# Performance work log

Measured on AMD Instinct MI355X. Metric: run time of the kernel, lower is better.

## Reference

```python
import jax, jax.numpy as jnp
import numpy as np
import math

B, T, F, H = 8, 1024, 512, 8
DK = F // H

def setup_inputs() -> dict:
    key = jax.random.key(0)
    ks = jax.random.split(key, 14)
    s = 0.02
    return {
        "query": jax.random.normal(ks[0], (B, T, F), jnp.float32),
        "key_in": jax.random.normal(ks[1], (B, T, F), jnp.float32),
        "value": jax.random.normal(ks[2], (B, T, F), jnp.float32),
        "pos_emb": jax.random.normal(ks[3], (1, 2 * T - 1, F), jnp.float32),
        "mask": jnp.ones((B, 1, T), jnp.int32),
        "Wq": jax.random.normal(ks[4], (F, F), jnp.float32) * s,
        "bq": jnp.zeros((F,), jnp.float32),
        "Wk": jax.random.normal(ks[5], (F, F), jnp.float32) * s,
        "bk": jnp.zeros((F,), jnp.float32),
        "Wv": jax.random.normal(ks[6], (F, F), jnp.float32) * s,
        "bv": jnp.zeros((F,), jnp.float32),
        "Wo": jax.random.normal(ks[7], (F, F), jnp.float32) * s,
        "bo": jnp.zeros((F,), jnp.float32),
        "Wp": jax.random.normal(ks[8], (F, F), jnp.float32) * s,
        "pos_bias_u": jax.random.normal(ks[9], (H, DK), jnp.float32) * s,
        "pos_bias_v": jax.random.normal(ks[10], (H, DK), jnp.float32) * s,
    }

def _rel_shift(x):
    # x: [B,H,T1, 2*T1-1] -> Transformer-XL pad/reshape trick -> [B,H,T1,T1]
    b, h, t1, n = x.shape
    zero_pad = jnp.zeros((b, h, t1, 1), x.dtype)
    x_padded = jnp.concatenate([zero_pad, x], axis=-1)  # [B,H,T1,n+1]
    x_padded = x_padded.reshape(b, h, n + 1, t1)
    x = x_padded[:, :, 1:].reshape(b, h, t1, n)
    return x[..., : n // 2 + 1]

def reference(query, key_in, value, pos_emb, mask,
              Wq, bq, Wk, bk, Wv, bv, Wo, bo, Wp, pos_bias_u, pos_bias_v):
    b, t1, f = query.shape
    # qkv projections -> [B,T,H,DK]
    q = (query @ Wq.T + bq).reshape(b, t1, H, DK)
    k = (key_in @ Wk.T + bk).reshape(b, -1, H, DK)
    v = (value @ Wv.T + bv).reshape(b, -1, H, DK)
    # positional projection (batch 1) -> [P,H,DK]
    p = (pos_emb @ Wp.T).reshape(pos_emb.shape[1], H, DK)
    q_u = q + pos_bias_u  # broadcast [H,DK]
    q_v = q + pos_bias_v
    matrix_ac = jnp.einsum("bthd,bshd->bhts", q_u, k)
    matrix_bd = jnp.einsum("bthd,phd->bhtp", q_v, p)
    matrix_bd = _rel_shift(matrix_bd)
    scores = (matrix_ac + matrix_bd) / math.sqrt(DK)  # [B,H,T,T]
    neg = jnp.finfo(scores.dtype).min
    m = (mask[:, None, :, :] == 0)  # [B,1,1,T] or [B,1,T,T]
    scores = jnp.where(m, neg, scores)
    attn = jax.nn.softmax(scores, axis=-1)
    attn = jnp.where(m, 0.0, attn)
    x = jnp.einsum("bhts,bshd->bthd", attn, v).reshape(b, t1, H * DK)
    return x @ Wo.T + bo
```

## Files before the change

### kernel.cpp

```cpp
#include <hip/hip_runtime.h>
#include <math.h>

#define T_SEQ 1024
#define FEAT  512
#define NH    8
#define DKH   64

typedef __attribute__((ext_vector_type(8))) short          bf16x8;
typedef _Float16 f16;
typedef __attribute__((ext_vector_type(8))) _Float16       f16x8;
typedef __attribute__((ext_vector_type(4))) float          f32x4;
typedef __attribute__((ext_vector_type(8))) unsigned short u16x8;
typedef __attribute__((ext_vector_type(4))) unsigned short u16x4;

__device__ __forceinline__ float bf2f(unsigned short u) {
    union { unsigned int i; float f; } x; x.i = ((unsigned int)u) << 16; return x.f;
}
__device__ __forceinline__ unsigned short f2bf(float f) {
    union { float f; unsigned int i; } x; x.f = f;
    unsigned int r = x.i + 0x7FFFu + ((x.i >> 16) & 1u);
    return (unsigned short)(r >> 16);
}
__device__ __forceinline__ unsigned short f2h_bits(float f) {
    const f16 h = (f16)f;
    union { f16 h; unsigned short u; } x; x.h = h; return x.u;
}

typedef const __attribute__((address_space(1))) unsigned int* gas_ptr;
typedef __attribute__((address_space(3))) unsigned int*       las_ptr;
__device__ __forceinline__ void glds16(const unsigned short* g, unsigned short* l) {
    __builtin_amdgcn_global_load_lds((gas_ptr)(const void*)g, (las_ptr)(void*)l, 16, 0, 0);
}

struct SplitPack {
    const float*    src[9];
    unsigned short* hi[9];
    unsigned short* lo[9];
    int             n4[9];
};

__global__ __launch_bounds__(256)
void split_f32(SplitPack pk) {
    const int ten = blockIdx.y;
    const int n4  = pk.n4[ten];
    const float4* s = (const float4*)pk.src[ten];
    u16x4* dh = (u16x4*)pk.hi[ten];
    u16x4* dl = (u16x4*)pk.lo[ten];
    for (int i = blockIdx.x * blockDim.x + threadIdx.x; i < n4;
         i += gridDim.x * blockDim.x) {
        const float4 v = s[i];
        float a[4] = {v.x, v.y, v.z, v.w};
        u16x4 h, l;
#pragma unroll
        for (int j = 0; j < 4; ++j) {
            h[j] = f2bf(a[j]);
            l[j] = f2bf(a[j] - bf2f(h[j]));
        }
        dh[i] = h; dl[i] = l;
    }
}

#define GBUF 12288

template<int OUTMODE>
__global__ __launch_bounds__(256)
void gemm_ps(const unsigned short* __restrict__ Agh,
             const unsigned short* __restrict__ Agl,
             const unsigned short* __restrict__ Wh,
             const unsigned short* __restrict__ Wl,
             const float* __restrict__ bias,
             void* __restrict__ Cout, int M, int N, int K)
{
    __shared__ unsigned short lds[2 * GBUF];

    const int tid  = threadIdx.x;
    const int w    = tid >> 6, lane = tid & 63, g = lane >> 4, c = lane & 15;
    const int m0   = blockIdx.x * 128, n0 = blockIdx.y * 64;
    const int wr   = (w >> 1) * 64, wc = (w & 1) * 32;

    f32x4 acc[4][2];
#pragma unroll
    for (int m = 0; m < 4; ++m)
#pragma unroll
        for (int n = 0; n < 2; ++n)
#pragma unroll
            for (int r = 0; r < 4; ++r) acc[m][n][r] = 0.f;

    auto STAGE = [&](unsigned short* base, int kc) {
        const int k0 = kc * 32;
#pragma unroll
        for (int q = 0; q < 2; ++q) {
            const int chunk = q * 256 + w * 64 + lane;
            const int row = chunk >> 2, p = chunk & 3;
            const int gra = m0 + row;
            const int gr  = (gra < M) ? gra : (M - 1);
            const size_t go = (size_t)gr * K + k0 + p * 8;
            glds16(Agh + go, base + chunk * 8);
            glds16(Agl + go, base + 4096 + chunk * 8);
        }
        {
            const int chunk = w * 64 + lane;
            const int row = chunk >> 2, p = chunk & 3;
            const size_t go = (size_t)(n0 + row) * K + k0 + p * 8;
            glds16(Wh + go, base + 8192 + chunk * 8);
            glds16(Wl + go, base + 10240 + chunk * 8);
        }
    };

    STAGE(lds, 0);
    __syncthreads();

    const int nk = K / 32;
    int cur = 0;
    for (int kc = 0; kc < nk; ++kc) {
        if (kc + 1 < nk) STAGE(lds + (cur ^ 1) * GBUF, kc + 1);

        const unsigned short* Bs = lds + cur * GBUF;
        bf16x8 ah[4], al[4], bh[2], bl[2];
#pragma unroll
        for (int m = 0; m < 4; ++m) {
            const int ro = (wr + 16 * m + c) * 32 + g * 8;
            ah[m] = *(const bf16x8*)&Bs[ro];
            al[m] = *(const bf16x8*)&Bs[4096 + ro];
        }
#pragma unroll
        for (int n = 0; n < 2; ++n) {
            const int ro = (wc + 16 * n + c) * 32 + g * 8;
            bh[n] = *(const bf16x8*)&Bs[8192 + ro];
            bl[n] = *(const bf16x8*)&Bs[10240 + ro];
        }
#pragma unroll
        for (int m = 0; m < 4; ++m)
#pragma unroll
            for (int n = 0; n < 2; ++n) {
                acc[m][n] = __builtin_amdgcn_mfma_f32_16x16x32_bf16(ah[m], bh[n], acc[m][n], 0, 0, 0);
                acc[m][n] = __builtin_amdgcn_mfma_f32_16x16x32_bf16(ah[m], bl[n], acc[m][n], 0, 0, 0);
                acc[m][n] = __builtin_amdgcn_mfma_f32_16x16x32_bf16(al[m], bh[n], acc[m][n], 0, 0, 0);
            }

        __syncthreads();
        cur ^= 1;
    }

#pragma unroll
    for (int n = 0; n < 2; ++n) {
        const int gcol = n0 + wc + 16 * n + c;
        const float bb = bias ? bias[gcol] : 0.f;
#pragma unroll
        for (int m = 0; m < 4; ++m) {
            if (OUTMODE == 2) {
                const int grb = m0 + wr + 16 * m + 4 * g;
                const int bidx = grb >> 10, t = grb & 1023;
                u16x4 pk4;
#pragma unroll
                for (int r = 0; r < 4; ++r) pk4[r] = f2h_bits(acc[m][n][r] + bb);
                *(u16x4*)&((unsigned short*)Cout)[((size_t)(bidx * FEAT + gcol)) * T_SEQ + t] = pk4;
            } else {
#pragma unroll
                for (int r = 0; r < 4; ++r) {
                    const int gr = m0 + wr + 16 * m + 4 * g + r;
                    if (gr < M) {
                        const float v = acc[m][n][r] + bb;
                        if (OUTMODE == 0) ((float*)Cout)[(size_t)gr * N + gcol] = v;
                        else ((unsigned short*)Cout)[(size_t)gr * N + gcol] = f2h_bits(v);
                    }
                }
            }
        }
    }
}

#define AST  72
#define BDST 132

__global__ __launch_bounds__(256)
void attn_f16(const unsigned short* __restrict__ qb,
              const unsigned short* __restrict__ kb,
              const unsigned short* __restrict__ vtg,
              const unsigned short* __restrict__ pb,
              const int* __restrict__ mask,
              const float* __restrict__ pbu, const float* __restrict__ pbv,
              unsigned short* __restrict__ xh, unsigned short* __restrict__ xl)
{
    extern __shared__ unsigned short sm[];
    unsigned short* kt  = sm;
    unsigned short* vtT = kt  + 64 * AST;
    unsigned short* pt  = vtT + 64 * AST;
    unsigned short* ps  = pt  + 128 * AST;
    unsigned short* bdb = ps  + 64 * AST;
    f16* bdf = (f16*)bdb;
    f16* psf = (f16*)ps;

    const int tid = threadIdx.x;
    const int w = tid >> 6, lane = tid & 63, g = lane >> 4, c = lane & 15;
    const int t0 = blockIdx.x * 64;
    const int b  = blockIdx.y >> 3, h = blockIdx.y & 7;

    const unsigned short* ksrc = kb + ((size_t)b * T_SEQ) * FEAT + h * DKH;
    const unsigned short* vsrc = vtg + ((size_t)(b * FEAT + h * DKH)) * T_SEQ;
    const unsigned short* psrc = pb + h * DKH;

    f16x8 aq0, aq1, av0, av1;
    {
        const unsigned short* qp =
            qb + ((size_t)(b * T_SEQ + t0 + 16 * w + c)) * FEAT + h * DKH + 8 * g;
        const f16x8 q0 = *(const f16x8*)qp;
        const f16x8 q1 = *(const f16x8*)(qp + 32);
        const float* pu = pbu + h * DKH + 8 * g;
        const float* pv = pbv + h * DKH + 8 * g;
#pragma unroll
        for (int j = 0; j < 8; ++j) {
            const float f0 = (float)q0[j], f1 = (float)q1[j];
            aq0[j] = (f16)(f0 + pu[j]);       av0[j] = (f16)(f0 + pv[j]);
            aq1[j] = (f16)(f1 + pu[j + 32]);  av1[j] = (f16)(f1 + pv[j + 32]);
        }
    }

    f32x4 accO[4];
    float m_r[4], l_r[4];
#pragma unroll
    for (int n = 0; n < 4; ++n)
#pragma unroll
        for (int r = 0; r < 4; ++r) accO[n][r] = 0.f;
#pragma unroll
    for (int r = 0; r < 4; ++r) { m_r[r] = -3.0e38f; l_r[r] = 0.f; }

    for (int st = 0; st < 16; ++st) {
        const int s0 = st * 64;
        const int pbase = (T_SEQ - DKH) - t0 + s0;
        __syncthreads();
#pragma unroll
        for (int q2 = 0; q2 < 2; ++q2) {
            const int id = tid + 256 * q2, row = id >> 3, chq = id & 7;
            *(u16x8*)&kt[row * AST + chq * 8] =
                *(const u16x8*)&ksrc[(size_t)(s0 + row) * FEAT + chq * 8];
            *(u16x8*)&vtT[row * AST + chq * 8] =
                *(const u16x8*)&vsrc[(size_t)row * T_SEQ + s0 + chq * 8];
        }
#pragma unroll
        for (int q2 = 0; q2 < 4; ++q2) {
            const int id = tid + 256 * q2, prow = id >> 3, chq = id & 7;
            u16x8 p8;
            if (prow < 127)
                p8 = *(const u16x8*)&psrc[(size_t)(pbase + prow) * FEAT + chq * 8];
            else {
#pragma unroll
                for (int j = 0; j < 8; ++j) p8[j] = 0;
            }
            *(u16x8*)&pt[prow * AST + chq * 8] = p8;
        }
        __syncthreads();

        f32x4 acS[4];
#pragma unroll
        for (int j = 0; j < 4; ++j)
#pragma unroll
            for (int r = 0; r < 4; ++r) acS[j][r] = 0.f;
#pragma unroll
        for (int j = 0; j < 4; ++j) {
            const f16x8 b0 = *(const f16x8*)&kt[(16 * j + c) * AST + 8 * g];
            const f16x8 b1 = *(const f16x8*)&kt[(16 * j + c) * AST + 32 + 8 * g];
            acS[j] = __builtin_amdgcn_mfma_f32_16x16x32_f16(aq0, b0, acS[j], 0, 0, 0);
            acS[j] = __builtin_amdgcn_mfma_f32_16x16x32_f16(aq1, b1, acS[j], 0, 0, 0);
        }

#pragma unroll
        for (int jj = 0; jj < 8; ++jj) {
            f32x4 bda;
#pragma unroll
            for (int r = 0; r < 4; ++r) bda[r] = 0.f;
            const f16x8 b0 = *(const f16x8*)&pt[(16 * jj + c) * AST + 8 * g];
            const f16x8 b1 = *(const f16x8*)&pt[(16 * jj + c) * AST + 32 + 8 * g];
            bda = __builtin_amdgcn_mfma_f32_16x16x32_f16(av0, b0, bda, 0, 0, 0);
            bda = __builtin_amdgcn_mfma_f32_16x16x32_f16(av1, b1, bda, 0, 0, 0);
#pragma unroll
            for (int r = 0; r < 4; ++r)
                bdf[(16 * w + 4 * g + r) * BDST + 16 * jj + c] = (f16)bda[r];
        }
        __syncthreads();

        int mk[4];
#pragma unroll
        for (int j = 0; j < 4; ++j) mk[j] = mask[b * T_SEQ + s0 + 16 * j + c];
#pragma unroll
        for (int r = 0; r < 4; ++r) {
            const int ti = 16 * w + 4 * g + r;
            float sv[4];
#pragma unroll
            for (int j = 0; j < 4; ++j) {
                const float bdv = (float)bdf[ti * BDST + (63 - ti + 16 * j + c)];
                sv[j] = (mk[j] == 0) ? -1.0e30f : (acS[j][r] + bdv) * 0.125f;
            }
            float mx = fmaxf(fmaxf(sv[0], sv[1]), fmaxf(sv[2], sv[3]));
            mx = fmaxf(mx, __shfl_xor(mx, 1)); mx = fmaxf(mx, __shfl_xor(mx, 2));
            mx = fmaxf(mx, __shfl_xor(mx, 4)); mx = fmaxf(mx, __shfl_xor(mx, 8));
            const float mnew = fmaxf(m_r[r], mx);
            const float corr = __expf(m_r[r] - mnew);
            m_r[r] = mnew;
            float rs = 0.f;
#pragma unroll
            for (int j = 0; j < 4; ++j) {
                const float e = (mk[j] == 0) ? 0.f : __expf(sv[j] - mnew);
                rs += e;
                psf[ti * AST + 16 * j + c] = (f16)e;
            }
            rs += __shfl_xor(rs, 1); rs += __shfl_xor(rs, 2);
            rs += __shfl_xor(rs, 4); rs += __shfl_xor(rs, 8);
            l_r[r] = l_r[r] * corr + rs;
#pragma unroll
            for (int n = 0; n < 4; ++n) accO[n][r] *= corr;
        }
        __syncthreads();

        const f16x8 pa0 = *(const f16x8*)&ps[(16 * w + c) * AST + 8 * g];
        const f16x8 pa1 = *(const f16x8*)&ps[(16 * w + c) * AST + 32 + 8 * g];
#pragma unroll
        for (int n = 0; n < 4; ++n) {
            const f16x8 b0 = *(const f16x8*)&vtT[(16 * n + c) * AST + 8 * g];
            const f16x8 b1 = *(const f16x8*)&vtT[(16 * n + c) * AST + 32 + 8 * g];
            accO[n] = __builtin_amdgcn_mfma_f32_16x16x32_f16(pa0, b0, accO[n], 0, 0, 0);
            accO[n] = __builtin_amdgcn_mfma_f32_16x16x32_f16(pa1, b1, accO[n], 0, 0, 0);
        }
    }

#pragma unroll
    for (int r = 0; r < 4; ++r) {
        const float inv = (l_r[r] > 0.f) ? 1.0f / l_r[r] : 0.f;
        const int t = t0 + 16 * w + 4 * g + r;
#pragma unroll
        for (int n = 0; n < 4; ++n) {
            const float xv = accO[n][r] * inv;
            const size_t idx = ((size_t)(b * T_SEQ + t)) * FEAT + h * DKH + 16 * n + c;
            const unsigned short hp = f2bf(xv);
            xh[idx] = hp;
            xl[idx] = f2bf(xv - bf2f(hp));
        }
    }
}

extern "C" void kernel_launch(void* const* d_in, const int* in_sizes, int n_in,
                              void* d_out, int out_size, void* d_ws, size_t ws_size,
                              hipStream_t stream)
{
    (void)in_sizes; (void)n_in; (void)out_size; (void)ws_size;
    const float* query   = (const float*)d_in[0];
    const float* key_in  = (const float*)d_in[1];
    const float* value   = (const float*)d_in[2];
    const float* pos_emb = (const float*)d_in[3];
    const int*   mask    = (const int*)  d_in[4];
    const float* Wq = (const float*)d_in[5];
    const float* bq = (const float*)d_in[6];
    const float* Wk = (const float*)d_in[7];
    const float* bk = (const float*)d_in[8];
    const float* Wv = (const float*)d_in[9];
    const float* bv = (const float*)d_in[10];
    const float* Wo = (const float*)d_in[11];
    const float* bo = (const float*)d_in[12];
    const float* Wp = (const float*)d_in[13];
    const float* pbu = (const float*)d_in[14];
    const float* pbv = (const float*)d_in[15];
    float* out = (float*)d_out;

    const size_t NTOK = (size_t)8 * T_SEQ;
    char* wsp = (char*)d_ws;
    size_t off = 0;
    auto alloc = [&](size_t bytes) { char* p = wsp + off; off += (bytes + 255) & ~255ull; return p; };

    unsigned short* qbf = (unsigned short*)alloc(NTOK * FEAT * 2);
    unsigned short* kbf = (unsigned short*)alloc(NTOK * FEAT * 2);
    unsigned short* vTb = (unsigned short*)alloc(NTOK * FEAT * 2);
    unsigned short* pbf = (unsigned short*)alloc((size_t)2047 * FEAT * 2);
    unsigned short* wh[5]; unsigned short* wl[5];
    for (int i = 0; i < 5; ++i) {
        wh[i] = (unsigned short*)alloc((size_t)FEAT * FEAT * 2);
        wl[i] = (unsigned short*)alloc((size_t)FEAT * FEAT * 2);
    }
    unsigned short* iqh = (unsigned short*)alloc(NTOK * FEAT * 2);
    unsigned short* iql = (unsigned short*)alloc(NTOK * FEAT * 2);
    unsigned short* ikh = (unsigned short*)alloc(NTOK * FEAT * 2);
    unsigned short* ikl = (unsigned short*)alloc(NTOK * FEAT * 2);
    unsigned short* ivh = (unsigned short*)alloc(NTOK * FEAT * 2);
    unsigned short* ivl = (unsigned short*)alloc(NTOK * FEAT * 2);
    unsigned short* iph = (unsigned short*)alloc((size_t)2047 * FEAT * 2);
    unsigned short* ipl = (unsigned short*)alloc((size_t)2047 * FEAT * 2);
    unsigned short* xh = iqh;
    unsigned short* xl = iql;

    SplitPack sp;
    const float* wsrc[9] = {Wq, Wk, Wv, Wp, Wo, query, key_in, value, pos_emb};
    unsigned short* hdst[9] = {wh[0], wh[1], wh[2], wh[3], wh[4], iqh, ikh, ivh, iph};
    unsigned short* ldst[9] = {wl[0], wl[1], wl[2], wl[3], wl[4], iql, ikl, ivl, ipl};
    for (int i = 0; i < 9; ++i) {
        sp.src[i] = wsrc[i]; sp.hi[i] = hdst[i]; sp.lo[i] = ldst[i];
        sp.n4[i] = (i < 5) ? (FEAT * FEAT / 4)
                           : ((i < 8) ? (int)(NTOK * FEAT / 4) : (2047 * FEAT / 4));
    }
    split_f32<<<dim3(256, 9), 256, 0, stream>>>(sp);

    gemm_ps<1><<<dim3(64, 8), 256, 0, stream>>>(iqh, iql, wh[0], wl[0], bq, qbf, 8192, FEAT, FEAT);
    gemm_ps<1><<<dim3(64, 8), 256, 0, stream>>>(ikh, ikl, wh[1], wl[1], bk, kbf, 8192, FEAT, FEAT);
    gemm_ps<2><<<dim3(64, 8), 256, 0, stream>>>(ivh, ivl, wh[2], wl[2], bv, vTb, 8192, FEAT, FEAT);
    gemm_ps<1><<<dim3(16, 8), 256, 0, stream>>>(iph, ipl, wh[3], wl[3], nullptr, pbf, 2047, FEAT, FEAT);

    const int lds_bytes = (64 * AST * 3 + 128 * AST + 64 * BDST) * 2;
    hipFuncSetAttribute((const void*)attn_f16,
                        hipFuncAttributeMaxDynamicSharedMemorySize, lds_bytes);
    attn_f16<<<dim3(16, 64), 256, lds_bytes, stream>>>(qbf, kbf, vTb, pbf,
                                                       mask, pbu, pbv, xh, xl);

    gemm_ps<0><<<dim3(64, 8), 256, 0, stream>>>(xh, xl, wh[4], wl[4], bo, out, 8192, FEAT, FEAT);
}
```

Measured before the change: 394.4 us.

## Compute rel-shift in registers via per-wave banded BD tiles and lane shuffles

Replaces the full 64x128 positional-score tile written to LDS and re-read with a shifted index. Each wave now computes only the five 16-wide BD blocks its diagonal band needs, keeps them in registers, and aligns the content scores with a lane shuffle plus a wrap select. Probabilities are written to LDS at the permuted column. This removes one LDS buffer, a block-wide barrier and the scattered f16 BD stores. In exchange it adds shuffles and extra accumulator registers, and the masked-entry test now relies on a sentinel threshold.

```diff
diff --git a/kernel.cpp b/kernel.cpp
--- a/kernel.cpp
+++ b/kernel.cpp
@@ -171,7 +171,6 @@
 }
 
 #define AST  72
-#define BDST 132
 
 __global__ __launch_bounds__(256)
 void attn_f16(const unsigned short* __restrict__ qb,
@@ -187,8 +186,6 @@
     unsigned short* vtT = kt  + 64 * AST;
     unsigned short* pt  = vtT + 64 * AST;
     unsigned short* ps  = pt  + 128 * AST;
-    unsigned short* bdb = ps  + 64 * AST;
-    f16* bdf = (f16*)bdb;
     f16* psf = (f16*)ps;
 
     const int tid = threadIdx.x;
@@ -264,32 +261,35 @@
             acS[j] = __builtin_amdgcn_mfma_f32_16x16x32_f16(aq1, b1, acS[j], 0, 0, 0);
         }
 
-#pragma unroll
-        for (int jj = 0; jj < 8; ++jj) {
-            f32x4 bda;
-#pragma unroll
-            for (int r = 0; r < 4; ++r) bda[r] = 0.f;
-            const f16x8 b0 = *(const f16x8*)&pt[(16 * jj + c) * AST + 8 * g];
-            const f16x8 b1 = *(const f16x8*)&pt[(16 * jj + c) * AST + 32 + 8 * g];
-            bda = __builtin_amdgcn_mfma_f32_16x16x32_f16(av0, b0, bda, 0, 0, 0);
-            bda = __builtin_amdgcn_mfma_f32_16x16x32_f16(av1, b1, bda, 0, 0, 0);
-#pragma unroll
-            for (int r = 0; r < 4; ++r)
-                bdf[(16 * w + 4 * g + r) * BDST + 16 * jj + c] = (f16)bda[r];
-        }
-        __syncthreads();
+        f32x4 bdacc[5];
+#pragma unroll
+        for (int q = 0; q < 5; ++q) {
+#pragma unroll
+            for (int r = 0; r < 4; ++r) bdacc[q][r] = 0.f;
+            const int prow = 16 * (q + 3 - w) + c;
+            const f16x8 b0 = *(const f16x8*)&pt[prow * AST + 8 * g];
+            const f16x8 b1 = *(const f16x8*)&pt[prow * AST + 32 + 8 * g];
+            bdacc[q] = __builtin_amdgcn_mfma_f32_16x16x32_f16(av0, b0, bdacc[q], 0, 0, 0);
+            bdacc[q] = __builtin_amdgcn_mfma_f32_16x16x32_f16(av1, b1, bdacc[q], 0, 0, 0);
+        }
 
         int mk[4];
 #pragma unroll
         for (int j = 0; j < 4; ++j) mk[j] = mask[b * T_SEQ + s0 + 16 * j + c];
 #pragma unroll
         for (int r = 0; r < 4; ++r) {
-            const int ti = 16 * w + 4 * g + r;
+            const int ti  = 16 * w + 4 * g + r;
+            const int dlt = 15 - 4 * g - r;
+            const int csh = (c - dlt) & 15;
+            const int src = (lane & 48) | csh;
+            const bool wrap = (c < dlt);
             float sv[4];
 #pragma unroll
             for (int j = 0; j < 4; ++j) {
-                const float bdv = (float)bdf[ti * BDST + (63 - ti + 16 * j + c)];
-                sv[j] = (mk[j] == 0) ? -1.0e30f : (acS[j][r] + bdv) * 0.125f;
+                const float acm = (mk[j] == 0) ? -1.0e30f : acS[j][r];
+                const float acf = __shfl(acm, src, 64);
+                const float bdv = wrap ? bdacc[j + 1][r] : bdacc[j][r];
+                sv[j] = (acf + bdv) * 0.125f;
             }
             float mx = fmaxf(fmaxf(sv[0], sv[1]), fmaxf(sv[2], sv[3]));
             mx = fmaxf(mx, __shfl_xor(mx, 1)); mx = fmaxf(mx, __shfl_xor(mx, 2));
@@ -300,9 +300,9 @@
             float rs = 0.f;
 #pragma unroll
             for (int j = 0; j < 4; ++j) {
-                const float e = (mk[j] == 0) ? 0.f : __expf(sv[j] - mnew);
+                const float e = (sv[j] < -1.0e28f) ? 0.f : __expf(sv[j] - mnew);
                 rs += e;
-                psf[ti * AST + 16 * j + c] = (f16)e;
+                psf[ti * AST + 16 * j + csh] = (f16)e;
             }
             rs += __shfl_xor(rs, 1); rs += __shfl_xor(rs, 2);
             rs += __shfl_xor(rs, 4); rs += __shfl_xor(rs, 8);
@@ -402,7 +402,7 @@
     gemm_ps<2><<<dim3(64, 8), 256, 0, stream>>>(ivh, ivl, wh[2], wl[2], bv, vTb, 8192, FEAT, FEAT);
     gemm_ps<1><<<dim3(16, 8), 256, 0, stream>>>(iph, ipl, wh[3], wl[3], nullptr, pbf, 2047, FEAT, FEAT);
 
-    const int lds_bytes = (64 * AST * 3 + 128 * AST + 64 * BDST) * 2;
+    const int lds_bytes = (64 * AST * 3 + 128 * AST) * 2;
     hipFuncSetAttribute((const void*)attn_f16,
                         hipFuncAttributeMaxDynamicSharedMemorySize, lds_bytes);
     attn_f16<<<dim3(16, 64), 256, lds_bytes, stream>>>(qbf, kbf, vTb, pbf,
```

Result: faster. 340.9 us (-13.6%).
